# Kernel tuning notes

Hardware: AMD Instinct MI355X
Metric: run time of the kernel (lower is better)

## Reference

```python
import jax, jax.numpy as jnp
import numpy as np

HEADS = 8
DIM_HEAD = 64
SCALE = DIM_HEAD ** -0.5


def setup_inputs() -> dict:
    key = jax.random.key(0)
    k1, k2, k3 = jax.random.split(key, 3)
    B, N, D = 4, 2048, 512
    inner = HEADS * DIM_HEAD  # 512
    x = jax.random.normal(k1, (B, N, D), dtype=jnp.float32)
    # nn.Linear stores weight [out, in]; y = x @ W.T
    w_qkv = jax.random.normal(k2, (3 * inner, D), dtype=jnp.float32) * (D ** -0.5)
    w_out = jax.random.normal(k3, (D, inner), dtype=jnp.float32) * (inner ** -0.5)
    b_out = jnp.zeros((D,), dtype=jnp.float32)
    return {"x": x, "w_qkv": w_qkv, "w_out": w_out, "b_out": b_out}


def reference(x, w_qkv, w_out, b_out):
    B, N, D = x.shape
    qkv = jnp.einsum('bnd,ed->bne', x, w_qkv)  # [B,N,3*inner]
    q, k, v = jnp.split(qkv, 3, axis=-1)
    def to_heads(t):
        return t.reshape(B, N, HEADS, DIM_HEAD).transpose(0, 2, 1, 3)  # [B,H,N,Dh]
    q, k, v = to_heads(q), to_heads(k), to_heads(v)
    dots = jnp.einsum('bhid,bhjd->bhij', q, k) * SCALE  # [B,H,N,N]
    attn = jax.nn.softmax(dots, axis=-1)
    out = jnp.einsum('bhij,bhjd->bhid', attn, v)  # [B,H,N,Dh]
    out = out.transpose(0, 2, 1, 3).reshape(B, N, HEADS * DIM_HEAD)
    return jnp.einsum('bne,de->bnd', out, w_out) + b_out
```

## Files before the change

### kernel.cpp

```cpp
#include <hip/hip_runtime.h>
#include <hip/hip_bf16.h>
#include <stdint.h>

typedef __bf16 bf16;
typedef __bf16 bf16x8 __attribute__((ext_vector_type(8)));
typedef __bf16 bf16x4 __attribute__((ext_vector_type(4)));
typedef float f32x4 __attribute__((ext_vector_type(4)));

template <int V> struct Int { static constexpr int value = V; };

static __device__ __forceinline__ void gl2lds16(const void* g, void* l) {
  const __attribute__((address_space(1))) void* gp =
      reinterpret_cast<const __attribute__((address_space(1))) void*>(
          reinterpret_cast<uintptr_t>(g));
  __attribute__((address_space(3))) void* lp =
      reinterpret_cast<__attribute__((address_space(3))) void*>(
          static_cast<uint32_t>(reinterpret_cast<uintptr_t>(l)));
  __builtin_amdgcn_global_load_lds(gp, lp, 16, 0, 0);
}

static __device__ __forceinline__ float fast_exp2(float x) {
#if __has_builtin(__builtin_amdgcn_exp2f)
  return __builtin_amdgcn_exp2f(x);
#else
  return exp2f(x);
#endif
}

__global__ __launch_bounds__(256) void cvt_all(const float* __restrict__ x,
                                               const float* __restrict__ wq,
                                               const float* __restrict__ wo,
                                               bf16* __restrict__ dst) {
  int i = blockIdx.x * 256 + threadIdx.x;
  const int stride = gridDim.x * 256;
  for (; i < 1310720; i += stride) {
    const float4 v = (i < 1048576) ? reinterpret_cast<const float4*>(x)[i]
                   : (i < 1245184) ? reinterpret_cast<const float4*>(wq)[i - 1048576]
                                   : reinterpret_cast<const float4*>(wo)[i - 1245184];
    bf16x4 o;
    o[0] = (bf16)v.x; o[1] = (bf16)v.y; o[2] = (bf16)v.z; o[3] = (bf16)v.w;
    reinterpret_cast<bf16x4*>(dst)[i] = o;
  }
}

__global__ __launch_bounds__(256) void qkv_gemm(const bf16* __restrict__ X,
                                                const bf16* __restrict__ W,
                                                bf16* __restrict__ Qb,
                                                bf16* __restrict__ Kb,
                                                bf16* __restrict__ Vt) {
  __shared__ __align__(16) bf16 AshX[8192];
  __shared__ __align__(16) bf16 BshX[8192];
  const int t = threadIdx.x;
  const int lane = t & 63;
  const int w = t >> 6;
  const int fr = lane & 15, fg = lane >> 4;
  const int wr = w >> 1, wc = w & 1;
  const int m0 = blockIdx.x * 128;
  const int n0 = blockIdx.y * 128;
  const int r0 = t >> 2, seg = t & 3;
  const bf16* pA0 = X + (m0 + r0) * 512 + seg * 8;
  const bf16* pA1 = X + (m0 + r0 + 64) * 512 + seg * 8;
  const bf16* pB0 = W + (n0 + r0) * 512 + seg * 8;
  const bf16* pB1 = W + (n0 + r0 + 64) * 512 + seg * 8;
  const bf16* ap = AshX + (wr * 64 + fr) * 32 + fg * 8;
  const bf16* bp = BshX + (wc * 64 + fr) * 32 + fg * 8;

  f32x4 acc[4][4] = {};

  auto stage = [&](auto Bt) {
    constexpr int B = decltype(Bt)::value;
    gl2lds16(pA0, (void*)(AshX + B * 4096 + t * 8));
    gl2lds16(pA1, (void*)(AshX + B * 4096 + 2048 + t * 8));
    gl2lds16(pB0, (void*)(BshX + B * 4096 + t * 8));
    gl2lds16(pB1, (void*)(BshX + B * 4096 + 2048 + t * 8));
    pA0 += 32; pA1 += 32; pB0 += 32; pB1 += 32;
  };
  auto step = [&](auto Bt) {
    constexpr int B = decltype(Bt)::value;
    bf16x8 a[4], b[4];
#pragma unroll
    for (int m = 0; m < 4; ++m) a[m] = *reinterpret_cast<const bf16x8*>(ap + B * 4096 + m * 512);
#pragma unroll
    for (int n = 0; n < 4; ++n) b[n] = *reinterpret_cast<const bf16x8*>(bp + B * 4096 + n * 512);
#pragma unroll
    for (int m = 0; m < 4; ++m)
#pragma unroll
      for (int n = 0; n < 4; ++n)
        acc[m][n] = __builtin_amdgcn_mfma_f32_16x16x32_bf16(a[m], b[n], acc[m][n], 0, 0, 0);
  };

  stage(Int<0>{});
  __syncthreads();
  for (int kt = 0; kt < 16; kt += 2) {
    stage(Int<1>{});
    step(Int<0>{});
    __syncthreads();
    if (kt < 14) stage(Int<0>{});
    step(Int<1>{});
    __syncthreads();
  }

  const int which = n0 >> 9;
#pragma unroll
  for (int n = 0; n < 4; ++n) {
    const int e = n0 + wc * 64 + 16 * n + fr;
    const int h = (e >> 6) & 7;
    const int d = e & 63;
#pragma unroll
    for (int m = 0; m < 4; ++m) {
      const int mbase = m0 + wr * 64 + 16 * m + fg * 4;
      if (which == 2) {
        bf16x4 pk;
#pragma unroll
        for (int r = 0; r < 4; ++r) pk[r] = (bf16)acc[m][n][r];
        const int b = mbase >> 11, tok = mbase & 2047;
        *reinterpret_cast<bf16x4*>(&Vt[((b * 8 + h) * 64 + d) * 2048 + tok]) = pk;
      } else {
        bf16* dst = (which == 0) ? Qb : Kb;
        const float sc = (which == 0) ? (0.125f * 1.44269504088896f) : 1.0f;
#pragma unroll
        for (int r = 0; r < 4; ++r) {
          const int row = mbase + r;
          const int b = row >> 11, tok = row & 2047;
          dst[((b * 8 + h) * 2048 + tok) * 64 + d] = (bf16)(acc[m][n][r] * sc);
        }
      }
    }
  }
}

__global__ __launch_bounds__(256, 2) void attn_fwd(const bf16* __restrict__ Qb,
                                                   const bf16* __restrict__ Kb,
                                                   const bf16* __restrict__ Vt,
                                                   bf16* __restrict__ Ob) {
  __shared__ __align__(16) bf16 sh[16384];
  const int t = threadIdx.x;
  const int lane = t & 63;
  const int w = t >> 6;
  const int fr = lane & 15, fg = lane >> 4;
  const int bh = blockIdx.x;
  const int q0 = blockIdx.y * 128 + 32 * w;

  const bf16* Qrow = Qb + (bh * 2048 + q0 + fr) * 64;
  const bf16x8 qa0 = *reinterpret_cast<const bf16x8*>(Qrow + fg * 8);
  const bf16x8 qa1 = *reinterpret_cast<const bf16x8*>(Qrow + 32 + fg * 8);
  const bf16x8 qb0 = *reinterpret_cast<const bf16x8*>(Qrow + 1024 + fg * 8);
  const bf16x8 qb1 = *reinterpret_cast<const bf16x8*>(Qrow + 1024 + 32 + fg * 8);

  bf16x8 ones;
#pragma unroll
  for (int i = 0; i < 8; ++i) ones[i] = (bf16)1.0f;

  const int c0row = t >> 3, cseg = t & 7;
  const int c1row = c0row + 32;
  const int s0 = (cseg ^ (c0row & 7)) * 8;
  const int s1 = (cseg ^ (c1row & 7)) * 8;
  const int kp0 = 32 * ((c0row >> 4) >> 1) + 8 * ((c0row & 15) >> 2) +
                  4 * ((c0row >> 4) & 1) + (c0row & 3);
  const int kp1 = 32 * ((c1row >> 4) >> 1) + 8 * ((c1row & 15) >> 2) +
                  4 * ((c1row >> 4) & 1) + (c1row & 3);
  const bf16* pK0 = Kb + bh * 131072 + kp0 * 64 + s0;
  const bf16* pK1 = Kb + bh * 131072 + kp1 * 64 + s1;
  const bf16* pV0 = Vt + bh * 131072 + c0row * 2048 + s0;
  const bf16* pV1 = Vt + bh * 131072 + c1row * 2048 + s1;

  const int swz = (fr & 7) << 4;
  const int ko0 = fr * 128 + ((fg * 16) ^ swz);
  const int ko1 = fr * 128 + ((64 + fg * 16) ^ swz);
  const char* shb = reinterpret_cast<const char*>(sh);

  f32x4 oA[4] = {}, oB[4] = {};
  f32x4 lA = {}, lB = {};
  const f32x4 fzero = {0.f, 0.f, 0.f, 0.f};

  auto stage = [&](auto St) {
    constexpr int S = decltype(St)::value;
    gl2lds16(pK0, (void*)(sh + S * 4096 + t * 8));
    gl2lds16(pK1, (void*)(sh + S * 4096 + 2048 + t * 8));
    gl2lds16(pV0, (void*)(sh + 8192 + S * 4096 + t * 8));
    gl2lds16(pV1, (void*)(sh + 8192 + S * 4096 + 2048 + t * 8));
    pK0 += 4096; pK1 += 4096; pV0 += 64; pV1 += 64;
  };

  auto compute = [&](auto St) {
    constexpr int S = decltype(St)::value;
    f32x4 sA[4], sB[4];
#pragma unroll
    for (int j = 0; j < 4; ++j) {
      const bf16x8 kf0 = *reinterpret_cast<const bf16x8*>(shb + ko0 + (S * 8192 + j * 2048));
      sA[j] = __builtin_amdgcn_mfma_f32_16x16x32_bf16(kf0, qa0, fzero, 0, 0, 0);
      sB[j] = __builtin_amdgcn_mfma_f32_16x16x32_bf16(kf0, qb0, fzero, 0, 0, 0);
      const bf16x8 kf1 = *reinterpret_cast<const bf16x8*>(shb + ko1 + (S * 8192 + j * 2048));
      sA[j] = __builtin_amdgcn_mfma_f32_16x16x32_bf16(kf1, qa1, sA[j], 0, 0, 0);
      sB[j] = __builtin_amdgcn_mfma_f32_16x16x32_bf16(kf1, qb1, sB[j], 0, 0, 0);
    }
    bf16x8 pA0, pB0;
#pragma unroll
    for (int j = 0; j < 2; ++j)
#pragma unroll
      for (int r = 0; r < 4; ++r) {
        pA0[4 * j + r] = (bf16)fast_exp2(sA[j][r]);
        pB0[4 * j + r] = (bf16)fast_exp2(sB[j][r]);
      }
    __builtin_amdgcn_s_setprio(1);
    lA = __builtin_amdgcn_mfma_f32_16x16x32_bf16(ones, pA0, lA, 0, 0, 0);
    lB = __builtin_amdgcn_mfma_f32_16x16x32_bf16(ones, pB0, lB, 0, 0, 0);
#pragma unroll
    for (int j = 0; j < 4; ++j) {
      const bf16x8 vf = *reinterpret_cast<const bf16x8*>(
          shb + ko0 + (16384 + S * 8192 + j * 2048));
      oA[j] = __builtin_amdgcn_mfma_f32_16x16x32_bf16(vf, pA0, oA[j], 0, 0, 0);
      oB[j] = __builtin_amdgcn_mfma_f32_16x16x32_bf16(vf, pB0, oB[j], 0, 0, 0);
    }
    __builtin_amdgcn_s_setprio(0);
    bf16x8 pA1, pB1;
#pragma unroll
    for (int j = 2; j < 4; ++j)
#pragma unroll
      for (int r = 0; r < 4; ++r) {
        pA1[4 * (j - 2) + r] = (bf16)fast_exp2(sA[j][r]);
        pB1[4 * (j - 2) + r] = (bf16)fast_exp2(sB[j][r]);
      }
    __builtin_amdgcn_s_setprio(1);
    lA = __builtin_amdgcn_mfma_f32_16x16x32_bf16(ones, pA1, lA, 0, 0, 0);
    lB = __builtin_amdgcn_mfma_f32_16x16x32_bf16(ones, pB1, lB, 0, 0, 0);
#pragma unroll
    for (int j = 0; j < 4; ++j) {
      const bf16x8 vf = *reinterpret_cast<const bf16x8*>(
          shb + ko1 + (16384 + S * 8192 + j * 2048));
      oA[j] = __builtin_amdgcn_mfma_f32_16x16x32_bf16(vf, pA1, oA[j], 0, 0, 0);
      oB[j] = __builtin_amdgcn_mfma_f32_16x16x32_bf16(vf, pB1, oB[j], 0, 0, 0);
    }
    __builtin_amdgcn_s_setprio(0);
  };

  stage(Int<0>{});
  __syncthreads();
  for (int kt = 0; kt < 32; kt += 2) {
    stage(Int<1>{});
    compute(Int<0>{});
    __syncthreads();
    if (kt < 30) stage(Int<0>{});
    compute(Int<1>{});
    __syncthreads();
  }

  const int b = bh >> 3, h = bh & 7;
  const int qA = q0 + fr;
  const float invA = 1.0f / lA[0];
  const float invB = 1.0f / lB[0];
#pragma unroll
  for (int j = 0; j < 4; ++j) {
    bf16x4 o4;
#pragma unroll
    for (int r = 0; r < 4; ++r) o4[r] = (bf16)(oA[j][r] * invA);
    *reinterpret_cast<bf16x4*>(&Ob[(b * 2048 + qA) * 512 + h * 64 + 16 * j + 4 * fg]) = o4;
#pragma unroll
    for (int r = 0; r < 4; ++r) o4[r] = (bf16)(oB[j][r] * invB);
    *reinterpret_cast<bf16x4*>(&Ob[(b * 2048 + qA + 16) * 512 + h * 64 + 16 * j + 4 * fg]) = o4;
  }
}

__global__ __launch_bounds__(256) void out_gemm(const bf16* __restrict__ O,
                                                const bf16* __restrict__ W,
                                                const float* __restrict__ bias,
                                                float* __restrict__ Y) {
  __shared__ __align__(16) bf16 Ash[2][64 * 32];
  __shared__ __align__(16) bf16 Bsh[2][64 * 32];
  const int t = threadIdx.x;
  const int lane = t & 63;
  const int w = t >> 6;
  const int fr = lane & 15, fg = lane >> 4;
  const int m0 = blockIdx.x * 64;
  const int n0 = blockIdx.y * 64;
  const int srow = t >> 2, sseg = t & 3;
  const bf16* gA = O + (m0 + srow) * 512 + sseg * 8;
  const bf16* gB = W + (n0 + srow) * 512 + sseg * 8;

  f32x4 acc[4] = {};
  gl2lds16(gA, &Ash[0][t * 8]);
  gl2lds16(gB, &Bsh[0][t * 8]);
  __syncthreads();
  int cur = 0;
  for (int kt = 0; kt < 16; ++kt) {
    if (kt < 15) {
      gl2lds16(gA + (kt + 1) * 32, &Ash[cur ^ 1][t * 8]);
      gl2lds16(gB + (kt + 1) * 32, &Bsh[cur ^ 1][t * 8]);
    }
    const bf16x8 a = *reinterpret_cast<const bf16x8*>(&Ash[cur][(16 * w + fr) * 32 + fg * 8]);
#pragma unroll
    for (int j = 0; j < 4; ++j) {
      const bf16x8 b = *reinterpret_cast<const bf16x8*>(&Bsh[cur][(16 * j + fr) * 32 + fg * 8]);
      acc[j] = __builtin_amdgcn_mfma_f32_16x16x32_bf16(a, b, acc[j], 0, 0, 0);
    }
    __syncthreads();
    cur ^= 1;
  }
  const int mbase = m0 + 16 * w + fg * 4;
#pragma unroll
  for (int j = 0; j < 4; ++j) {
    const int col = n0 + 16 * j + fr;
    const float bv = bias[col];
#pragma unroll
    for (int r = 0; r < 4; ++r) {
      Y[(mbase + r) * 512 + col] = acc[j][r] + bv;
    }
  }
}

extern "C" void kernel_launch(void* const* d_in, const int* in_sizes, int n_in,
                              void* d_out, int out_size, void* d_ws, size_t ws_size,
                              hipStream_t stream) {
  const float* x = (const float*)d_in[0];
  const float* w_qkv = (const float*)d_in[1];
  const float* w_out = (const float*)d_in[2];
  const float* b_out = (const float*)d_in[3];
  float* y = (float*)d_out;
  char* ws = (char*)d_ws;
  bf16* xb    = (bf16*)(ws);
  bf16* wqkvb = (bf16*)(ws + 8388608);
  bf16* woutb = (bf16*)(ws + 9961472);
  bf16* Qb    = (bf16*)(ws + 10485760);
  bf16* Kb    = (bf16*)(ws + 18874368);
  bf16* Vt    = (bf16*)(ws + 27262976);
  bf16* Ob    = (bf16*)(ws + 35651584);

  hipLaunchKernelGGL(cvt_all, dim3(5120), dim3(256), 0, stream, x, w_qkv, w_out, xb);
  hipLaunchKernelGGL(qkv_gemm, dim3(64, 12), dim3(256), 0, stream, xb, wqkvb, Qb, Kb, Vt);
  hipLaunchKernelGGL(attn_fwd, dim3(32, 16), dim3(256), 0, stream, Qb, Kb, Vt, Ob);
  hipLaunchKernelGGL(out_gemm, dim3(128, 8), dim3(256), 0, stream, Ob, woutb, b_out, y);
}
```

Before: 76.94 us.

## Enlarge output GEMM tile to 128x128 with 4x4 MFMA per warp

The output projection GEMM moves from 64x64 tiles, where each warp does one 16-row strip, to 128x128 tiles split as a 2x2 grid of warps, each computing a 64x64 sub-tile with 16 MFMA accumulators. The k-loop is unrolled by two with compile-time buffer indices for double buffering. The aim is more MFMA work per LDS load and less global re-fetch of A and B. In exchange the grid shrinks from 1024 to 256 blocks, and register use rises, which may reduce occupancy.

```diff
diff --git a/kernel.cpp b/kernel.cpp
--- a/kernel.cpp
+++ b/kernel.cpp
@@ -265,45 +265,69 @@
                                                 const bf16* __restrict__ W,
                                                 const float* __restrict__ bias,
                                                 float* __restrict__ Y) {
-  __shared__ __align__(16) bf16 Ash[2][64 * 32];
-  __shared__ __align__(16) bf16 Bsh[2][64 * 32];
+  __shared__ __align__(16) bf16 Ash[8192];
+  __shared__ __align__(16) bf16 Bsh[8192];
   const int t = threadIdx.x;
   const int lane = t & 63;
   const int w = t >> 6;
   const int fr = lane & 15, fg = lane >> 4;
-  const int m0 = blockIdx.x * 64;
-  const int n0 = blockIdx.y * 64;
-  const int srow = t >> 2, sseg = t & 3;
-  const bf16* gA = O + (m0 + srow) * 512 + sseg * 8;
-  const bf16* gB = W + (n0 + srow) * 512 + sseg * 8;
-
-  f32x4 acc[4] = {};
-  gl2lds16(gA, &Ash[0][t * 8]);
-  gl2lds16(gB, &Bsh[0][t * 8]);
+  const int wr = w >> 1, wc = w & 1;
+  const int m0 = blockIdx.x * 128;
+  const int n0 = blockIdx.y * 128;
+  const int r0 = t >> 2, seg = t & 3;
+  const bf16* pA0 = O + (m0 + r0) * 512 + seg * 8;
+  const bf16* pA1 = O + (m0 + r0 + 64) * 512 + seg * 8;
+  const bf16* pB0 = W + (n0 + r0) * 512 + seg * 8;
+  const bf16* pB1 = W + (n0 + r0 + 64) * 512 + seg * 8;
+  const bf16* ap = Ash + (wr * 64 + fr) * 32 + fg * 8;
+  const bf16* bp = Bsh + (wc * 64 + fr) * 32 + fg * 8;
+
+  f32x4 acc[4][4] = {};
+
+  auto stage = [&](auto Bt) {
+    constexpr int B = decltype(Bt)::value;
+    gl2lds16(pA0, (void*)(Ash + B * 4096 + t * 8));
+    gl2lds16(pA1, (void*)(Ash + B * 4096 + 2048 + t * 8));
+    gl2lds16(pB0, (void*)(Bsh + B * 4096 + t * 8));
+    gl2lds16(pB1, (void*)(Bsh + B * 4096 + 2048 + t * 8));
+    pA0 += 32; pA1 += 32; pB0 += 32; pB1 += 32;
+  };
+  auto step = [&](auto Bt) {
+    constexpr int B = decltype(Bt)::value;
+    bf16x8 a[4], b[4];
+#pragma unroll
+    for (int m = 0; m < 4; ++m) a[m] = *reinterpret_cast<const bf16x8*>(ap + B * 4096 + m * 512);
+#pragma unroll
+    for (int n = 0; n < 4; ++n) b[n] = *reinterpret_cast<const bf16x8*>(bp + B * 4096 + n * 512);
+#pragma unroll
+    for (int m = 0; m < 4; ++m)
+#pragma unroll
+      for (int n = 0; n < 4; ++n)
+        acc[m][n] = __builtin_amdgcn_mfma_f32_16x16x32_bf16(a[m], b[n], acc[m][n], 0, 0, 0);
+  };
+
+  stage(Int<0>{});
   __syncthreads();
-  int cur = 0;
-  for (int kt = 0; kt < 16; ++kt) {
-    if (kt < 15) {
-      gl2lds16(gA + (kt + 1) * 32, &Ash[cur ^ 1][t * 8]);
-      gl2lds16(gB + (kt + 1) * 32, &Bsh[cur ^ 1][t * 8]);
-    }
-    const bf16x8 a = *reinterpret_cast<const bf16x8*>(&Ash[cur][(16 * w + fr) * 32 + fg * 8]);
-#pragma unroll
-    for (int j = 0; j < 4; ++j) {
-      const bf16x8 b = *reinterpret_cast<const bf16x8*>(&Bsh[cur][(16 * j + fr) * 32 + fg * 8]);
-      acc[j] = __builtin_amdgcn_mfma_f32_16x16x32_bf16(a, b, acc[j], 0, 0, 0);
-    }
-    __syncthreads();
-    cur ^= 1;
-  }
-  const int mbase = m0 + 16 * w + fg * 4;
-#pragma unroll
-  for (int j = 0; j < 4; ++j) {
-    const int col = n0 + 16 * j + fr;
+  for (int kt = 0; kt < 16; kt += 2) {
+    stage(Int<1>{});
+    step(Int<0>{});
+    __syncthreads();
+    if (kt < 14) stage(Int<0>{});
+    step(Int<1>{});
+    __syncthreads();
+  }
+
+#pragma unroll
+  for (int n = 0; n < 4; ++n) {
+    const int col = n0 + wc * 64 + 16 * n + fr;
     const float bv = bias[col];
 #pragma unroll
-    for (int r = 0; r < 4; ++r) {
-      Y[(mbase + r) * 512 + col] = acc[j][r] + bv;
+    for (int m = 0; m < 4; ++m) {
+      const int mbase = m0 + wr * 64 + 16 * m + fg * 4;
+#pragma unroll
+      for (int r = 0; r < 4; ++r) {
+        Y[(mbase + r) * 512 + col] = acc[m][n][r] + bv;
+      }
     }
   }
 }
@@ -328,5 +352,5 @@
   hipLaunchKernelGGL(cvt_all, dim3(5120), dim3(256), 0, stream, x, w_qkv, w_out, xb);
   hipLaunchKernelGGL(qkv_gemm, dim3(64, 12), dim3(256), 0, stream, xb, wqkvb, Qb, Kb, Vt);
   hipLaunchKernelGGL(attn_fwd, dim3(32, 16), dim3(256), 0, stream, Qb, Kb, Vt, Ob);
-  hipLaunchKernelGGL(out_gemm, dim3(128, 8), dim3(256), 0, stream, Ob, woutb, b_out, y);
-}
+  hipLaunchKernelGGL(out_gemm, dim3(64, 4), dim3(256), 0, stream, Ob, woutb, b_out, y);
+}
```

New measurement: 78.97 us. 2.6% more time.

## Split KV range across two wave groups per attention block with LDS reduction

Applied to the files above, without the earlier changes.

Doubles the attention block to 512 threads, with two groups of four waves each processing half of the key/value sequence for the same queries. The partial outputs and row sums from group 1 are written to LDS and added by group 0 before normalization, which works because the softmax uses no running max. This doubles the waves in flight to better hide latency on an under-occupied grid, at the cost of double the LDS per block, an extra barrier, and a reduction step.

```diff
diff --git a/kernel.cpp b/kernel.cpp
--- a/kernel.cpp
+++ b/kernel.cpp
@@ -129,17 +129,19 @@
   }
 }
 
-__global__ __launch_bounds__(256, 2) void attn_fwd(const bf16* __restrict__ Qb,
+__global__ __launch_bounds__(512, 4) void attn_fwd(const bf16* __restrict__ Qb,
                                                    const bf16* __restrict__ Kb,
                                                    const bf16* __restrict__ Vt,
                                                    bf16* __restrict__ Ob) {
-  __shared__ __align__(16) bf16 sh[16384];
+  __shared__ __align__(16) bf16 sh[32768];
   const int t = threadIdx.x;
   const int lane = t & 63;
   const int w = t >> 6;
+  const int g = w >> 2;
+  const int wl = w & 3;
   const int fr = lane & 15, fg = lane >> 4;
   const int bh = blockIdx.x;
-  const int q0 = blockIdx.y * 128 + 32 * w;
+  const int q0 = blockIdx.y * 128 + 32 * wl;
 
   const bf16* Qrow = Qb + (bh * 2048 + q0 + fr) * 64;
   const bf16x8 qa0 = *reinterpret_cast<const bf16x8*>(Qrow + fg * 8);
@@ -151,7 +153,8 @@
 #pragma unroll
   for (int i = 0; i < 8; ++i) ones[i] = (bf16)1.0f;
 
-  const int c0row = t >> 3, cseg = t & 7;
+  const int tg = t & 255;
+  const int c0row = tg >> 3, cseg = tg & 7;
   const int c1row = c0row + 32;
   const int s0 = (cseg ^ (c0row & 7)) * 8;
   const int s1 = (cseg ^ (c1row & 7)) * 8;
@@ -159,15 +162,17 @@
                   4 * ((c0row >> 4) & 1) + (c0row & 3);
   const int kp1 = 32 * ((c1row >> 4) >> 1) + 8 * ((c1row & 15) >> 2) +
                   4 * ((c1row >> 4) & 1) + (c1row & 3);
-  const bf16* pK0 = Kb + bh * 131072 + kp0 * 64 + s0;
-  const bf16* pK1 = Kb + bh * 131072 + kp1 * 64 + s1;
-  const bf16* pV0 = Vt + bh * 131072 + c0row * 2048 + s0;
-  const bf16* pV1 = Vt + bh * 131072 + c1row * 2048 + s1;
-
+  const int kvbase = g * 1024;
+  const bf16* pK0 = Kb + bh * 131072 + (kvbase + kp0) * 64 + s0;
+  const bf16* pK1 = Kb + bh * 131072 + (kvbase + kp1) * 64 + s1;
+  const bf16* pV0 = Vt + bh * 131072 + c0row * 2048 + kvbase + s0;
+  const bf16* pV1 = Vt + bh * 131072 + c1row * 2048 + kvbase + s1;
+
+  bf16* ar = sh + g * 16384;
+  const char* shb = reinterpret_cast<const char*>(sh) + g * 32768;
   const int swz = (fr & 7) << 4;
   const int ko0 = fr * 128 + ((fg * 16) ^ swz);
   const int ko1 = fr * 128 + ((64 + fg * 16) ^ swz);
-  const char* shb = reinterpret_cast<const char*>(sh);
 
   f32x4 oA[4] = {}, oB[4] = {};
   f32x4 lA = {}, lB = {};
@@ -175,10 +180,10 @@
 
   auto stage = [&](auto St) {
     constexpr int S = decltype(St)::value;
-    gl2lds16(pK0, (void*)(sh + S * 4096 + t * 8));
-    gl2lds16(pK1, (void*)(sh + S * 4096 + 2048 + t * 8));
-    gl2lds16(pV0, (void*)(sh + 8192 + S * 4096 + t * 8));
-    gl2lds16(pV1, (void*)(sh + 8192 + S * 4096 + 2048 + t * 8));
+    gl2lds16(pK0, (void*)(ar + S * 4096 + tg * 8));
+    gl2lds16(pK1, (void*)(ar + S * 4096 + 2048 + tg * 8));
+    gl2lds16(pV0, (void*)(ar + 8192 + S * 4096 + tg * 8));
+    gl2lds16(pV1, (void*)(ar + 8192 + S * 4096 + 2048 + tg * 8));
     pK0 += 4096; pK1 += 4096; pV0 += 64; pV1 += 64;
   };
 
@@ -236,28 +241,47 @@
 
   stage(Int<0>{});
   __syncthreads();
-  for (int kt = 0; kt < 32; kt += 2) {
+  for (int kt = 0; kt < 16; kt += 2) {
     stage(Int<1>{});
     compute(Int<0>{});
     __syncthreads();
-    if (kt < 30) stage(Int<0>{});
+    if (kt < 14) stage(Int<0>{});
     compute(Int<1>{});
     __syncthreads();
   }
 
-  const int b = bh >> 3, h = bh & 7;
-  const int qA = q0 + fr;
-  const float invA = 1.0f / lA[0];
-  const float invB = 1.0f / lB[0];
-#pragma unroll
-  for (int j = 0; j < 4; ++j) {
-    bf16x4 o4;
-#pragma unroll
-    for (int r = 0; r < 4; ++r) o4[r] = (bf16)(oA[j][r] * invA);
-    *reinterpret_cast<bf16x4*>(&Ob[(b * 2048 + qA) * 512 + h * 64 + 16 * j + 4 * fg]) = o4;
-#pragma unroll
-    for (int r = 0; r < 4; ++r) o4[r] = (bf16)(oB[j][r] * invB);
-    *reinterpret_cast<bf16x4*>(&Ob[(b * 2048 + qA + 16) * 512 + h * 64 + 16 * j + 4 * fg]) = o4;
+  if (g == 1) {
+    float* dst = reinterpret_cast<float*>(sh) + (wl * 64 + lane) * 34;
+#pragma unroll
+    for (int j = 0; j < 4; ++j) {
+      *reinterpret_cast<f32x4*>(dst + 4 * j) = oA[j];
+      *reinterpret_cast<f32x4*>(dst + 16 + 4 * j) = oB[j];
+    }
+    dst[32] = lA[0];
+    dst[33] = lB[0];
+  }
+  __syncthreads();
+  if (g == 0) {
+    const float* src = reinterpret_cast<const float*>(sh) + (wl * 64 + lane) * 34;
+#pragma unroll
+    for (int j = 0; j < 4; ++j) {
+      oA[j] += *reinterpret_cast<const f32x4*>(src + 4 * j);
+      oB[j] += *reinterpret_cast<const f32x4*>(src + 16 + 4 * j);
+    }
+    const float invA = 1.0f / (lA[0] + src[32]);
+    const float invB = 1.0f / (lB[0] + src[33]);
+    const int b = bh >> 3, h = bh & 7;
+    const int qA = q0 + fr;
+#pragma unroll
+    for (int j = 0; j < 4; ++j) {
+      bf16x4 o4;
+#pragma unroll
+      for (int r = 0; r < 4; ++r) o4[r] = (bf16)(oA[j][r] * invA);
+      *reinterpret_cast<bf16x4*>(&Ob[(b * 2048 + qA) * 512 + h * 64 + 16 * j + 4 * fg]) = o4;
+#pragma unroll
+      for (int r = 0; r < 4; ++r) o4[r] = (bf16)(oB[j][r] * invB);
+      *reinterpret_cast<bf16x4*>(&Ob[(b * 2048 + qA + 16) * 512 + h * 64 + 16 * j + 4 * fg]) = o4;
+    }
   }
 }
 
@@ -327,6 +351,6 @@
 
   hipLaunchKernelGGL(cvt_all, dim3(5120), dim3(256), 0, stream, x, w_qkv, w_out, xb);
   hipLaunchKernelGGL(qkv_gemm, dim3(64, 12), dim3(256), 0, stream, xb, wqkvb, Qb, Kb, Vt);
-  hipLaunchKernelGGL(attn_fwd, dim3(32, 16), dim3(256), 0, stream, Qb, Kb, Vt, Ob);
+  hipLaunchKernelGGL(attn_fwd, dim3(32, 16), dim3(512), 0, stream, Qb, Kb, Vt, Ob);
   hipLaunchKernelGGL(out_gemm, dim3(128, 8), dim3(256), 0, stream, Ob, woutb, b_out, y);
 }
```

Result: slower. 81.61 us (+6.1%).

## Fuse fp32-to-bf16 conversion of x into the QKV GEMM load path

Applied to the files above, without the earlier changes.

The separate conversion of the 16 MB fp32 activation x into a bf16 workspace is removed. The QKV GEMM now streams fp32 x tiles straight into LDS with an XOR swizzle and converts them to bf16 in registers before the MFMA. Only the weights are still converted by a smaller pre-pass. This drops a full write and read of the bf16 copy of x, but each GEMM block now loads twice as many A bytes from global memory, uses more LDS, and does extra conversion work in the inner loop.

```diff
diff --git a/kernel.cpp b/kernel.cpp
--- a/kernel.cpp
+++ b/kernel.cpp
@@ -27,28 +27,23 @@
 #endif
 }
 
-__global__ __launch_bounds__(256) void cvt_all(const float* __restrict__ x,
-                                               const float* __restrict__ wq,
-                                               const float* __restrict__ wo,
-                                               bf16* __restrict__ dst) {
-  int i = blockIdx.x * 256 + threadIdx.x;
-  const int stride = gridDim.x * 256;
-  for (; i < 1310720; i += stride) {
-    const float4 v = (i < 1048576) ? reinterpret_cast<const float4*>(x)[i]
-                   : (i < 1245184) ? reinterpret_cast<const float4*>(wq)[i - 1048576]
-                                   : reinterpret_cast<const float4*>(wo)[i - 1245184];
-    bf16x4 o;
-    o[0] = (bf16)v.x; o[1] = (bf16)v.y; o[2] = (bf16)v.z; o[3] = (bf16)v.w;
-    reinterpret_cast<bf16x4*>(dst)[i] = o;
-  }
-}
-
-__global__ __launch_bounds__(256) void qkv_gemm(const bf16* __restrict__ X,
+__global__ __launch_bounds__(256) void cvt_w(const float* __restrict__ wq,
+                                             const float* __restrict__ wo,
+                                             bf16* __restrict__ dst) {
+  const int i = blockIdx.x * 256 + threadIdx.x;
+  const float4 v = (i < 196608) ? reinterpret_cast<const float4*>(wq)[i]
+                                : reinterpret_cast<const float4*>(wo)[i - 196608];
+  bf16x4 o;
+  o[0] = (bf16)v.x; o[1] = (bf16)v.y; o[2] = (bf16)v.z; o[3] = (bf16)v.w;
+  reinterpret_cast<bf16x4*>(dst)[i] = o;
+}
+
+__global__ __launch_bounds__(256) void qkv_gemm(const float* __restrict__ X,
                                                 const bf16* __restrict__ W,
                                                 bf16* __restrict__ Qb,
                                                 bf16* __restrict__ Kb,
                                                 bf16* __restrict__ Vt) {
-  __shared__ __align__(16) bf16 AshX[8192];
+  __shared__ __align__(16) float AshF[8192];
   __shared__ __align__(16) bf16 BshX[8192];
   const int t = threadIdx.x;
   const int lane = t & 63;
@@ -57,29 +52,40 @@
   const int wr = w >> 1, wc = w & 1;
   const int m0 = blockIdx.x * 128;
   const int n0 = blockIdx.y * 128;
+  const float* pA = X + (m0 + (t >> 3)) * 512 + ((t & 7) ^ ((t >> 3) & 7)) * 4;
   const int r0 = t >> 2, seg = t & 3;
-  const bf16* pA0 = X + (m0 + r0) * 512 + seg * 8;
-  const bf16* pA1 = X + (m0 + r0 + 64) * 512 + seg * 8;
   const bf16* pB0 = W + (n0 + r0) * 512 + seg * 8;
   const bf16* pB1 = W + (n0 + r0 + 64) * 512 + seg * 8;
-  const bf16* ap = AshX + (wr * 64 + fr) * 32 + fg * 8;
+  const char* af = reinterpret_cast<const char*>(AshF);
+  const int koa0 = (wr * 64 + fr) * 128 + (((fg * 2) ^ (fr & 7)) * 16);
+  const int koa1 = (wr * 64 + fr) * 128 + (((fg * 2 + 1) ^ (fr & 7)) * 16);
   const bf16* bp = BshX + (wc * 64 + fr) * 32 + fg * 8;
 
   f32x4 acc[4][4] = {};
 
   auto stage = [&](auto Bt) {
     constexpr int B = decltype(Bt)::value;
-    gl2lds16(pA0, (void*)(AshX + B * 4096 + t * 8));
-    gl2lds16(pA1, (void*)(AshX + B * 4096 + 2048 + t * 8));
+    gl2lds16(pA,         (void*)(AshF + B * 4096 + t * 4));
+    gl2lds16(pA + 16384, (void*)(AshF + B * 4096 + 1024 + t * 4));
+    gl2lds16(pA + 32768, (void*)(AshF + B * 4096 + 2048 + t * 4));
+    gl2lds16(pA + 49152, (void*)(AshF + B * 4096 + 3072 + t * 4));
     gl2lds16(pB0, (void*)(BshX + B * 4096 + t * 8));
     gl2lds16(pB1, (void*)(BshX + B * 4096 + 2048 + t * 8));
-    pA0 += 32; pA1 += 32; pB0 += 32; pB1 += 32;
+    pA += 32; pB0 += 32; pB1 += 32;
   };
   auto step = [&](auto Bt) {
     constexpr int B = decltype(Bt)::value;
     bf16x8 a[4], b[4];
 #pragma unroll
-    for (int m = 0; m < 4; ++m) a[m] = *reinterpret_cast<const bf16x8*>(ap + B * 4096 + m * 512);
+    for (int m = 0; m < 4; ++m) {
+      const f32x4 a0 = *reinterpret_cast<const f32x4*>(af + B * 16384 + m * 2048 + koa0);
+      const f32x4 a1 = *reinterpret_cast<const f32x4*>(af + B * 16384 + m * 2048 + koa1);
+#pragma unroll
+      for (int i = 0; i < 4; ++i) {
+        a[m][i] = (bf16)a0[i];
+        a[m][4 + i] = (bf16)a1[i];
+      }
+    }
 #pragma unroll
     for (int n = 0; n < 4; ++n) b[n] = *reinterpret_cast<const bf16x8*>(bp + B * 4096 + n * 512);
 #pragma unroll
@@ -317,7 +323,6 @@
   const float* b_out = (const float*)d_in[3];
   float* y = (float*)d_out;
   char* ws = (char*)d_ws;
-  bf16* xb    = (bf16*)(ws);
   bf16* wqkvb = (bf16*)(ws + 8388608);
   bf16* woutb = (bf16*)(ws + 9961472);
   bf16* Qb    = (bf16*)(ws + 10485760);
@@ -325,8 +330,8 @@
   bf16* Vt    = (bf16*)(ws + 27262976);
   bf16* Ob    = (bf16*)(ws + 35651584);
 
-  hipLaunchKernelGGL(cvt_all, dim3(5120), dim3(256), 0, stream, x, w_qkv, w_out, xb);
-  hipLaunchKernelGGL(qkv_gemm, dim3(64, 12), dim3(256), 0, stream, xb, wqkvb, Qb, Kb, Vt);
+  hipLaunchKernelGGL(cvt_w, dim3(1024), dim3(256), 0, stream, w_qkv, w_out, wqkvb);
+  hipLaunchKernelGGL(qkv_gemm, dim3(64, 12), dim3(256), 0, stream, x, wqkvb, Qb, Kb, Vt);
   hipLaunchKernelGGL(attn_fwd, dim3(32, 16), dim3(256), 0, stream, Qb, Kb, Vt, Ob);
   hipLaunchKernelGGL(out_gemm, dim3(128, 8), dim3(256), 0, stream, Ob, woutb, b_out, y);
 }
```

New measurement: 80.80 us. 5.0% more time.
